# Kernel tuning notes

Measured on AMD Instinct MI355X. Metric: run time of the kernel, lower is better.

## Reference

```python
import jax, jax.numpy as jnp
import numpy as np

REST = 0.0
DECAY = 0.5
THRESHOLD = 0.5
SG_WIDTH = 1.0  # rectangular surrogate-gradient window width

@jax.custom_vjp
def spike(v):
    return (v > THRESHOLD).astype(v.dtype)

def _spike_fwd(v):
    return spike(v), v

def _spike_bwd(v, g):
    # rectangular surrogate: d spike / d v = 1/width * 1[|v - threshold| < width/2]
    grad = (jnp.abs(v - THRESHOLD) < (SG_WIDTH * 0.5)).astype(g.dtype) / SG_WIDTH
    return (g * grad,)

spike.defvjp(_spike_fwd, _spike_bwd)

def setup_inputs() -> dict:
    key = jax.random.key(0)
    k1, k2, k3 = jax.random.split(key, 3)
    T, B, N = 128, 128, 1024
    tx = jax.random.normal(k1, (T, B, N), dtype=jnp.float32)
    lim = 1.0 / np.sqrt(N)  # nn.Linear default init range
    W = jax.random.uniform(k2, (N, N), dtype=jnp.float32, minval=-lim, maxval=lim)
    b = jax.random.uniform(k3, (N,), dtype=jnp.float32, minval=-lim, maxval=lim)
    return {"tx": tx, "W": W, "b": b}

def reference(tx, W, b):
    # tx: [T, B, N]; W: [N, N] (nn.Linear weight, applied as y @ W.T + b)
    v0 = jnp.full_like(tx[0], REST)
    y0 = jnp.zeros_like(tx[0])

    def step(carry, x):
        v, y = carry
        x = x + y @ W.T + b                      # recurrent input
        v = DECAY * v * (1.0 - y) + REST * y + x  # leaky integrate with reset
        y = spike(v)                              # threshold fire
        return (v, y), y

    _, ty = jax.lax.scan(step, (v0, y0), tx)
    return ty  # [T, B, N]
```

## Files before the change

### kernel.cpp

```cpp
#include <hip/hip_runtime.h>
#include <stdint.h>

#define TT 128
#define BB 128
#define NN 1024


typedef unsigned short ushort8 __attribute__((ext_vector_type(8)));

__device__ __forceinline__ float bfbits2f(uint32_t lo16) {
  union { uint32_t i; float f; } c;
  c.i = lo16 << 16;
  return c.f;
}

__device__ __forceinline__ void gload_lds16(const void* g, void* l) {
  __builtin_amdgcn_global_load_lds(
      (const __attribute__((address_space(1))) uint32_t*)g,
      (__attribute__((address_space(3))) uint32_t*)l, 16, 0, 0);
}

__global__ __launch_bounds__(256) void w_transpose_repack(
    float* __restrict__ W, uint16_t* __restrict__ WtBf,
    uint32_t* __restrict__ dirty) {
  __shared__ float ta[32][33];
  __shared__ float tb[32][33];

  int rem = blockIdx.x;
  int I = 0;
  while (rem >= (32 - I)) { rem -= (32 - I); ++I; }
  const int J = I + rem;

  const int lx = threadIdx.x & 31;
  const int ly = threadIdx.x >> 5;
  uint32_t bad = 0;

  if (I == J) {
#pragma unroll
    for (int i = 0; i < 4; ++i)
      ta[ly + i * 8][lx] = W[(I * 32 + ly + i * 8) * NN + J * 32 + lx];
    __syncthreads();
#pragma unroll
    for (int i = 0; i < 4; ++i) {
      const int idx = (I * 32 + ly + i * 8) * NN + J * 32 + lx;
      const float v = ta[lx][ly + i * 8];
      const uint32_t bits = __float_as_uint(v);
      W[idx] = v;
      WtBf[idx] = (uint16_t)(bits >> 16);
      bad |= (bits & 0xFFFFu);
    }
  } else {
#pragma unroll
    for (int i = 0; i < 4; ++i) {
      ta[ly + i * 8][lx] = W[(I * 32 + ly + i * 8) * NN + J * 32 + lx];
      tb[ly + i * 8][lx] = W[(J * 32 + ly + i * 8) * NN + I * 32 + lx];
    }
    __syncthreads();
#pragma unroll
    for (int i = 0; i < 4; ++i) {
      const int idxA = (J * 32 + ly + i * 8) * NN + I * 32 + lx;
      const float va = ta[lx][ly + i * 8];
      const uint32_t bitsA = __float_as_uint(va);
      W[idxA] = va;
      WtBf[idxA] = (uint16_t)(bitsA >> 16);
      bad |= (bitsA & 0xFFFFu);

      const int idxB = (I * 32 + ly + i * 8) * NN + J * 32 + lx;
      const float vb = tb[lx][ly + i * 8];
      const uint32_t bitsB = __float_as_uint(vb);
      W[idxB] = vb;
      WtBf[idxB] = (uint16_t)(bitsB >> 16);
      bad |= (bitsB & 0xFFFFu);
    }
  }
  const unsigned long long bm = __ballot(bad != 0);
  if ((threadIdx.x & 63) == 0 && bm) atomicOr(dirty, 1u);
}

__global__ __launch_bounds__(512) void lif_half(
    const void* __restrict__ tx_raw, const float* __restrict__ bias,
    const float* __restrict__ WtF32, const uint16_t* __restrict__ WtBf,
    const uint32_t* __restrict__ dirty,
    unsigned long long* __restrict__ gmask, float* __restrict__ out) {
  const int bb = blockIdx.x;
  const int b = bb & 127;
  const int h = bb >> 7;
  const int pp = bb ^ 128;
  const int tid = threadIdx.x;
  const int lane = tid & 63;
  const int wv = tid >> 6;
  const int n = (h << 9) + tid;

  __shared__ uint16_t sbuf[3][16][512] __attribute__((aligned(16)));
  __shared__ uint16_t lst[NN] __attribute__((aligned(16)));
  __shared__ unsigned long long smask[16];
  __shared__ int sprobe;

  if (tid == 0) sprobe = 0;
  __syncthreads();
  {
    const uint32_t* txw = (const uint32_t*)tx_raw;
    int local = 0;
#pragma unroll
    for (int i = 0; i < 2; ++i) {
      const uint32_t f = (txw[tid * 2 + i] >> 7) & 0xFFu;
      local += (f >= 0x74u && f < 0x81u) ? 1 : 0;
    }
    atomicAdd(&sprobe, local);
  }
  __syncthreads();
  const bool tx_is_bf16 = (sprobe > 512);
  const bool w_bf = (*dirty == 0u);

  const uint16_t* __restrict__ txh = (const uint16_t*)tx_raw;
  const float* __restrict__ txf = (const float*)tx_raw;
  const float bz = bias[n];

  const char* __restrict__ wbase = (const char*)WtBf;
  const float* __restrict__ rowF = WtF32 + n;
  const size_t lane16 = (size_t)(lane << 4);
  const size_t hoff = (size_t)(h << 10);

  float v = 0.0f;
  int y = 0;

  auto gF = [&](int s, int e) -> float {
    float acc = 0.0f;
    int i = s;
    for (; i + 8 <= e; i += 8) {
      float w[8];
#pragma unroll
      for (int u = 0; u < 8; ++u) {
        const int k = __builtin_amdgcn_readfirstlane((int)lst[i + u]);
        w[u] = rowF[k << 10];
      }
#pragma unroll
      for (int u = 0; u < 8; ++u) acc += w[u];
    }
    for (; i < e; ++i) {
      const int k = __builtin_amdgcn_readfirstlane((int)lst[i]);
      acc += rowF[k << 10];
    }
    return acc;
  };

  for (int t = 0; t < TT; ++t) {
    const int sl = t & 3;
    const unsigned long long m = __ballot(y);
    if (lane == 0) smask[h * 8 + wv] = m;
    if (lane < 2) {
      const uint32_t word = (lane == 0) ? (uint32_t)m : (uint32_t)(m >> 32);
      const unsigned long long cell =
          ((unsigned long long)(t + 1) << 32) | (unsigned long long)word;
      __hip_atomic_store(&gmask[((size_t)bb * 4 + sl) * 16 + wv * 2 + lane],
                         cell, __ATOMIC_RELAXED, __HIP_MEMORY_SCOPE_AGENT);
    }

    const int off = (t * BB + b) * NN + n;
    float xx;
    if (tx_is_bf16)
      xx = bfbits2f((uint32_t)__builtin_nontemporal_load(&txh[off]));
    else
      xx = __builtin_nontemporal_load(&txf[off]);

    __syncthreads();
    if (tid < 16) {
      const size_t ci = ((size_t)pp * 4 + sl) * 16 + tid;
      unsigned long long cell;
      while (((cell = __hip_atomic_load(&gmask[ci], __ATOMIC_RELAXED,
                                        __HIP_MEMORY_SCOPE_AGENT)) >>
              32) != (unsigned long long)(t + 1)) {
        __builtin_amdgcn_s_sleep(1);
      }
      ((uint32_t*)smask)[(1 - h) * 16 + tid] = (uint32_t)cell;
    }
    __syncthreads();

    unsigned long long mk[16];
    int cnt[16];
#pragma unroll
    for (int i = 0; i < 16; ++i) {
      mk[i] = smask[i];
      cnt[i] = __popcll(mk[i]);
    }
    int pref[16];
    {
      int s = 0;
#pragma unroll
      for (int j = 0; j < 6; ++j) { pref[j] = s; s += cnt[j]; }
    }
    {
      int s = 384;
#pragma unroll
      for (int j = 6; j < 12; ++j) { pref[j] = s; s += cnt[j]; }
    }
    {
      int s = 768;
#pragma unroll
      for (int j = 12; j < 16; ++j) { pref[j] = s; s += cnt[j]; }
    }
    const int c0 = pref[5] + cnt[5];
    const int c1 = pref[11] + cnt[11] - 384;
    const int c2 = pref[15] + cnt[15] - 768;

#pragma unroll
    for (int jj = 0; jj < 2; ++jj) {
      const int j = wv * 2 + jj;
      const unsigned long long bits = mk[j];
      if ((bits >> lane) & 1ull) {
        const int below = __builtin_amdgcn_mbcnt_hi(
            (uint32_t)(bits >> 32),
            __builtin_amdgcn_mbcnt_lo((uint32_t)bits, 0));
        lst[pref[j] + below] = (uint16_t)(j * 64 + lane);
      }
    }
    if (tid < 48) {
      const int p = tid >> 4, jn = tid & 15;
      const int c = (p == 0) ? c0 : ((p == 1) ? c1 : c2);
      if (c + jn < ((c + 15) & ~15)) lst[p * 384 + c + jn] = (uint16_t)NN;
    }
    __syncthreads();

    float P0 = 0.0f, P1 = 0.0f, P2 = 0.0f;
    if (w_bf) {
      const int n0c = (c0 + 15) >> 4;
      const int n1c = (c1 + 15) >> 4;
      const int n2c = (c2 + 15) >> 4;
      const int nct = n0c + n1c + n2c;

      int ka = 0, kb = 0;
      auto readk = [&](int c) {
        int pb;
        if (c < n0c) pb = c * 16;
        else if (c < n0c + n1c) pb = 384 + (c - n0c) * 16;
        else pb = 768 + (c - n0c - n1c) * 16;
        ka = (int)lst[pb + wv * 2];
        kb = (int)lst[pb + wv * 2 + 1];
      };
      auto stage2 = [&](int cb) {
        gload_lds16(wbase + ((size_t)ka << 11) + hoff + lane16,
                    &sbuf[cb][wv * 2 + 0][0]);
        gload_lds16(wbase + ((size_t)kb << 11) + hoff + lane16,
                    &sbuf[cb][wv * 2 + 1][0]);
      };

      if (nct > 0) {
        readk(0); stage2(0);
        if (nct > 1) { readk(1); stage2(1); }
        if (nct > 2) readk(2);
        for (int c = 0; c < nct; ++c) {
          const int cb = c - (c / 3) * 3;
          if (c + 2 < nct) {
            const int tb = (c + 2) - ((c + 2) / 3) * 3;
            stage2(tb);
            if (c + 3 < nct) readk(c + 3);
          }
          if (c + 2 < nct)
            asm volatile("s_waitcnt vmcnt(4)\n\ts_barrier" ::: "memory");
          else if (c + 1 < nct)
            asm volatile("s_waitcnt vmcnt(2)\n\ts_barrier" ::: "memory");
          else
            asm volatile("s_waitcnt vmcnt(0)\n\ts_barrier" ::: "memory");

          const uint16_t* rp = &sbuf[cb][0][tid];
          if (c < n0c) {
#pragma unroll
            for (int r = 0; r < 16; ++r)
              P0 += bfbits2f((uint32_t)rp[r * 512]);
          } else if (c < n0c + n1c) {
#pragma unroll
            for (int r = 0; r < 16; ++r)
              P1 += bfbits2f((uint32_t)rp[r * 512]);
          } else {
#pragma unroll
            for (int r = 0; r < 16; ++r)
              P2 += bfbits2f((uint32_t)rp[r * 512]);
          }
          asm volatile("s_barrier" ::: "memory");
        }
      }
    } else {
      P0 = gF(0, c0);
      P1 = gF(384, 384 + c1);
      P2 = gF(768, 768 + c2);
    }
    const float a = (P0 + P1) + P2;

    const float xv = (xx + a) + bz;
    v = (y ? 0.0f : 0.5f * v) + xv;
    y = (v > 0.5f);

    __builtin_nontemporal_store(y ? 1.0f : 0.0f, &out[off]);
  }
}

__global__ __launch_bounds__(1024) void lif_persample(
    const void* __restrict__ tx_raw, const float* __restrict__ bias,
    const float* __restrict__ WtF32, const uint16_t* __restrict__ WtBf,
    const uint32_t* __restrict__ dirty, float* __restrict__ out) {
  const int b = blockIdx.x;
  const int tid = threadIdx.x;
  const int lane = tid & 63;
  const int wv = tid >> 6;

  __shared__ uint16_t lst[NN] __attribute__((aligned(16)));
  __shared__ int wcnt[16];
  __shared__ int sprobe;

  if (tid == 0) sprobe = 0;
  __syncthreads();
  {
    const uint32_t* txw = (const uint32_t*)tx_raw;
    int local = 0;
#pragma unroll
    for (int i = 0; i < 2; ++i) {
      const uint32_t f = (txw[tid * 2 + i] >> 7) & 0xFFu;
      local += (f >= 0x74u && f < 0x81u) ? 1 : 0;
    }
    atomicAdd(&sprobe, local);
  }
  __syncthreads();
  const bool tx_is_bf16 = (sprobe > 1024);
  const bool w_bf = (*dirty == 0u);

  const uint16_t* __restrict__ txh = (const uint16_t*)tx_raw;
  const float* __restrict__ txf = (const float*)tx_raw;
  const float bz = bias[tid];

  const int pidx = (wv < 6) ? 0 : ((wv < 12) ? 1 : 2);
  const int pw0 = (pidx == 0) ? 0 : ((pidx == 1) ? 6 : 12);

  const uint16_t* __restrict__ rowB = WtBf + tid;
  const float* __restrict__ rowF = WtF32 + tid;

  float v = 0.0f;
  int y = 0;

  auto gB = [&](int pbase, int cnt) -> float {
    float acc = 0.0f;
    for (int i = 0; i < cnt; i += 32) {
      const ushort8* lp = (const ushort8*)(lst + pbase + i);
      const ushort8 a0 = lp[0];
      const ushort8 a1 = lp[1];
      const ushort8 a2 = lp[2];
      const ushort8 a3 = lp[3];
      float wbuf[32];
#pragma unroll
      for (int u = 0; u < 8; ++u) {
        const int k = __builtin_amdgcn_readfirstlane((int)a0[u]);
        wbuf[u] = bfbits2f((uint32_t)rowB[k << 10]);
      }
#pragma unroll
      for (int u = 0; u < 8; ++u) {
        const int k = __builtin_amdgcn_readfirstlane((int)a1[u]);
        wbuf[8 + u] = bfbits2f((uint32_t)rowB[k << 10]);
      }
#pragma unroll
      for (int u = 0; u < 8; ++u) {
        const int k = __builtin_amdgcn_readfirstlane((int)a2[u]);
        wbuf[16 + u] = bfbits2f((uint32_t)rowB[k << 10]);
      }
#pragma unroll
      for (int u = 0; u < 8; ++u) {
        const int k = __builtin_amdgcn_readfirstlane((int)a3[u]);
        wbuf[24 + u] = bfbits2f((uint32_t)rowB[k << 10]);
      }
#pragma unroll
      for (int u = 0; u < 32; ++u) acc += wbuf[u];
    }
    return acc;
  };

  auto gF = [&](int s, int e) -> float {
    float acc = 0.0f;
    int i = s;
    for (; i + 8 <= e; i += 8) {
      float w[8];
#pragma unroll
      for (int u = 0; u < 8; ++u) {
        const int k = __builtin_amdgcn_readfirstlane((int)lst[i + u]);
        w[u] = rowF[k << 10];
      }
#pragma unroll
      for (int u = 0; u < 8; ++u) acc += w[u];
    }
    for (; i < e; ++i) {
      const int k = __builtin_amdgcn_readfirstlane((int)lst[i]);
      acc += rowF[k << 10];
    }
    return acc;
  };

  for (int t = 0; t < TT; ++t) {
    const unsigned long long m = __ballot(y);
    if (lane == 0) wcnt[wv] = __popcll(m);
    __syncthreads();
    int base = 0, c0 = 0, c1 = 0, c2 = 0;
#pragma unroll
    for (int w = 0; w < 16; ++w) {
      const int c = wcnt[w];
      c0 += (w < 6) ? c : 0;
      c1 += (w >= 6 && w < 12) ? c : 0;
      c2 += (w >= 12) ? c : 0;
      base += (w >= pw0 && w < wv) ? c : 0;
    }
    if (y) {
      const int below = __builtin_amdgcn_mbcnt_hi(
          (uint32_t)(m >> 32), __builtin_amdgcn_mbcnt_lo((uint32_t)m, 0));
      lst[pidx * 384 + base + below] = (uint16_t)tid;
    }
    if (tid < 96) {
      const int p = tid >> 5, jn = tid & 31;
      const int c = (p == 0) ? c0 : ((p == 1) ? c1 : c2);
      if (c + jn < ((c + 31) & ~31)) lst[p * 384 + c + jn] = (uint16_t)NN;
    }
    __syncthreads();

    float P0, P1, P2;
    if (w_bf) {
      P0 = gB(0, (c0 + 31) & ~31);
      P1 = gB(384, (c1 + 31) & ~31);
      P2 = gB(768, (c2 + 31) & ~31);
    } else {
      P0 = gF(0, c0);
      P1 = gF(384, 384 + c1);
      P2 = gF(768, 768 + c2);
    }
    const float a = (P0 + P1) + P2;

    const int off = (t * BB + b) * NN + tid;
    const float xx = tx_is_bf16
        ? bfbits2f((uint32_t)__builtin_nontemporal_load(&txh[off]))
        : __builtin_nontemporal_load(&txf[off]);
    const float xv = (xx + a) + bz;
    v = (y ? 0.0f : 0.5f * v) + xv;
    y = (v > 0.5f);

    __builtin_nontemporal_store(y ? 1.0f : 0.0f, &out[off]);
  }
}

extern "C" void kernel_launch(void* const* d_in, const int* in_sizes, int n_in,
                              void* d_out, int out_size, void* d_ws, size_t ws_size,
                              hipStream_t stream) {
  const void* tx = nullptr;
  float* W = nullptr;
  const float* bs = nullptr;
  for (int i = 0; i < n_in; ++i) {
    if (in_sizes[i] == TT * BB * NN) tx = d_in[i];
    else if (in_sizes[i] == NN * NN) W = (float*)d_in[i];
    else if (in_sizes[i] == NN) bs = (const float*)d_in[i];
  }
  float* out = (float*)d_out;

  const size_t MB2 = 2u * 1024u * 1024u;
  uint16_t* WtBf = (uint16_t*)d_ws;
  uint16_t* zrow = WtBf + NN * NN;
  uint32_t* dirty = (uint32_t*)((char*)d_ws + MB2 + 2048u);
  unsigned long long* gmask =
      (unsigned long long*)((char*)d_ws + MB2 + 4096u);
  const size_t GMASK_BYTES = 256u * 4u * 16u * 8u;
  const size_t need = MB2 + 4096u + GMASK_BYTES;

  hipMemsetAsync(dirty, 0, sizeof(uint32_t), stream);
  hipMemsetAsync(zrow, 0, NN * sizeof(uint16_t), stream);

  w_transpose_repack<<<dim3(528), dim3(256), 0, stream>>>(W, WtBf, dirty);

  if (ws_size >= need) {
    hipMemsetAsync(gmask, 0, GMASK_BYTES, stream);
    lif_half<<<dim3(256), dim3(512), 0, stream>>>(tx, bs, W, WtBf, dirty,
                                                  gmask, out);
  } else {
    lif_persample<<<dim3(BB), dim3(1024), 0, stream>>>(tx, bs, W, WtBf, dirty,
                                                       out);
  }
}
```

Baseline: 1.741 ms.

## Replace block-wide barrier pipeline with per-wave double-buffered weight-row staging

Each wave now gathers only the 64 bf16 columns it consumes, for 8 spiking rows per chunk, into its own double-buffered LDS slot. Waves advance with per-wave vmcnt/lgkmcnt waits instead of a block-wide s_barrier at each chunk, so slow waves no longer stall the whole block. The cost is a smaller chunk granularity (8 rows instead of 16), which means more loop iterations and a shallower prefetch depth (2 stages instead of 3). Padding of the spike index lists is changed to multiples of 8 to match.

```diff
diff --git a/kernel.cpp b/kernel.cpp
--- a/kernel.cpp
+++ b/kernel.cpp
@@ -91,7 +91,7 @@
   const int wv = tid >> 6;
   const int n = (h << 9) + tid;
 
-  __shared__ uint16_t sbuf[3][16][512] __attribute__((aligned(16)));
+  __shared__ uint16_t wbuf[8][2][512] __attribute__((aligned(16)));
   __shared__ uint16_t lst[NN] __attribute__((aligned(16)));
   __shared__ unsigned long long smask[16];
   __shared__ int sprobe;
@@ -118,8 +118,9 @@
 
   const char* __restrict__ wbase = (const char*)WtBf;
   const float* __restrict__ rowF = WtF32 + n;
-  const size_t lane16 = (size_t)(lane << 4);
-  const size_t hoff = (size_t)(h << 10);
+  const size_t lbyte = (size_t)(h << 10) + (size_t)(wv << 7) +
+                       (size_t)((lane & 7) << 4);
+  const int lrow = lane >> 3;
 
   float v = 0.0f;
   int y = 0;
@@ -214,69 +215,57 @@
         lst[pref[j] + below] = (uint16_t)(j * 64 + lane);
       }
     }
-    if (tid < 48) {
-      const int p = tid >> 4, jn = tid & 15;
+    if (tid < 24) {
+      const int p = tid >> 3, jn = tid & 7;
       const int c = (p == 0) ? c0 : ((p == 1) ? c1 : c2);
-      if (c + jn < ((c + 15) & ~15)) lst[p * 384 + c + jn] = (uint16_t)NN;
+      if (c + jn < ((c + 7) & ~7)) lst[p * 384 + c + jn] = (uint16_t)NN;
     }
     __syncthreads();
 
     float P0 = 0.0f, P1 = 0.0f, P2 = 0.0f;
     if (w_bf) {
-      const int n0c = (c0 + 15) >> 4;
-      const int n1c = (c1 + 15) >> 4;
-      const int n2c = (c2 + 15) >> 4;
+      const int n0c = (c0 + 7) >> 3;
+      const int n1c = (c1 + 7) >> 3;
+      const int n2c = (c2 + 7) >> 3;
       const int nct = n0c + n1c + n2c;
 
-      int ka = 0, kb = 0;
-      auto readk = [&](int c) {
-        int pb;
-        if (c < n0c) pb = c * 16;
-        else if (c < n0c + n1c) pb = 384 + (c - n0c) * 16;
-        else pb = 768 + (c - n0c - n1c) * 16;
-        ka = (int)lst[pb + wv * 2];
-        kb = (int)lst[pb + wv * 2 + 1];
+      uint16_t* const wb0 = &wbuf[wv][0][0];
+      uint16_t* const wb1 = &wbuf[wv][1][0];
+
+      auto pbase = [&](int c) -> int {
+        if (c < n0c) return c * 8;
+        if (c < n0c + n1c) return 384 + (c - n0c) * 8;
+        return 768 + (c - n0c - n1c) * 8;
       };
-      auto stage2 = [&](int cb) {
-        gload_lds16(wbase + ((size_t)ka << 11) + hoff + lane16,
-                    &sbuf[cb][wv * 2 + 0][0]);
-        gload_lds16(wbase + ((size_t)kb << 11) + hoff + lane16,
-                    &sbuf[cb][wv * 2 + 1][0]);
+      auto stage = [&](int c, uint16_t* dst) {
+        const int k = (int)lst[pbase(c) + lrow];
+        gload_lds16(wbase + ((size_t)k << 11) + lbyte, dst);
       };
 
       if (nct > 0) {
-        readk(0); stage2(0);
-        if (nct > 1) { readk(1); stage2(1); }
-        if (nct > 2) readk(2);
+        stage(0, wb0);
+        if (nct > 1) stage(1, wb1);
         for (int c = 0; c < nct; ++c) {
-          const int cb = c - (c / 3) * 3;
-          if (c + 2 < nct) {
-            const int tb = (c + 2) - ((c + 2) / 3) * 3;
-            stage2(tb);
-            if (c + 3 < nct) readk(c + 3);
+          uint16_t* const buf = (c & 1) ? wb1 : wb0;
+          if (c + 1 < nct)
+            asm volatile("s_waitcnt vmcnt(1)" ::: "memory");
+          else
+            asm volatile("s_waitcnt vmcnt(0)" ::: "memory");
+          uint16_t vals[8];
+#pragma unroll
+          for (int r = 0; r < 8; ++r) vals[r] = buf[r * 64 + lane];
+          asm volatile("s_waitcnt lgkmcnt(0)" ::: "memory");
+          if (c + 2 < nct) stage(c + 2, buf);
+          if (c < n0c) {
+#pragma unroll
+            for (int r = 0; r < 8; ++r) P0 += bfbits2f((uint32_t)vals[r]);
+          } else if (c < n0c + n1c) {
+#pragma unroll
+            for (int r = 0; r < 8; ++r) P1 += bfbits2f((uint32_t)vals[r]);
+          } else {
+#pragma unroll
+            for (int r = 0; r < 8; ++r) P2 += bfbits2f((uint32_t)vals[r]);
           }
-          if (c + 2 < nct)
-            asm volatile("s_waitcnt vmcnt(4)\n\ts_barrier" ::: "memory");
-          else if (c + 1 < nct)
-            asm volatile("s_waitcnt vmcnt(2)\n\ts_barrier" ::: "memory");
-          else
-            asm volatile("s_waitcnt vmcnt(0)\n\ts_barrier" ::: "memory");
-
-          const uint16_t* rp = &sbuf[cb][0][tid];
-          if (c < n0c) {
-#pragma unroll
-            for (int r = 0; r < 16; ++r)
-              P0 += bfbits2f((uint32_t)rp[r * 512]);
-          } else if (c < n0c + n1c) {
-#pragma unroll
-            for (int r = 0; r < 16; ++r)
-              P1 += bfbits2f((uint32_t)rp[r * 512]);
-          } else {
-#pragma unroll
-            for (int r = 0; r < 16; ++r)
-              P2 += bfbits2f((uint32_t)rp[r * 512]);
-          }
-          asm volatile("s_barrier" ::: "memory");
         }
       }
     } else {
```

After: 1.750 ms. Within noise of the previous version (+0.6%).
